# Performance work log

Measured on AMD Instinct MI355X. Metric: run time of the kernel, lower is better.

## Reference

```python
import jax, jax.numpy as jnp
import numpy as np

B, T, L, IN, D, H = 2, 16, 256, 768, 1024, 16
HD = D // H
NREG = 4
P = NREG + 2          # frozen prefix: registers + noise + action
DEPTH = 8
TINT = 4              # temporal_attention_interval
CTX = 30              # temporal_context_length
BASE = 1000.0         # rope_base
EPS = 1e-6            # qk_norm_eps / rmsnorm eps
HID = 4096            # 4.0 * latent_dim
S = L + P             # tokens per frame


def _rms(x, w=None, eps=EPS):
    y = x * jax.lax.rsqrt(jnp.mean(x * x, axis=-1, keepdims=True) + eps)
    return y * w if w is not None else y


def _rope_cache(n, hd, base):
    inv = base ** (-jnp.arange(0, hd, 2, dtype=jnp.float32) / hd)
    ang = jnp.arange(n, dtype=jnp.float32)[:, None] * inv[None, :]  # [n, hd/2]
    return jnp.cos(ang), jnp.sin(ang)


def _apply_rope(x, cos, sin):
    x1, x2 = x[..., ::2], x[..., 1::2]
    return jnp.stack([x1 * cos - x2 * sin, x1 * sin + x2 * cos], axis=-1).reshape(x.shape)


def _attn(x, Wqkv, Wo, cos, sin, mask):
    # x: [..., S, D]; mask: bool, True = attend, broadcastable to [..., H, S, S]
    qkv = x @ Wqkv
    q, k, v = jnp.split(qkv, 3, axis=-1)
    heads = lambda t: t.reshape(t.shape[:-1] + (H, HD)).swapaxes(-2, -3)  # [..., H, S, HD]
    q, k, v = heads(q), heads(k), heads(v)
    q = _apply_rope(_rms(q), cos, sin)   # qk-norm then RoPE
    k = _apply_rope(_rms(k), cos, sin)
    s = jnp.einsum('...qd,...kd->...qk', q, k) / jnp.sqrt(jnp.float32(HD))
    s = jnp.where(mask, s, jnp.float32(-1e9))
    p = jax.nn.softmax(s, axis=-1) * mask.any(axis=-1, keepdims=True)  # zero rows with no allowed keys
    o = jnp.einsum('...qk,...kd->...qd', p, v)
    return o.swapaxes(-2, -3).reshape(x.shape) @ Wo


def _spatial_mask():
    m = np.zeros((S, S), bool)
    r, n, a, ls = NREG, NREG, NREG + 1, NREG + 2
    m[ls:, ls:] = True; m[ls:, n] = True; m[ls:, a] = True; m[ls:, :r] = True
    m[n, n] = True; m[a, a] = True
    m[:r, ls:] = True; m[:r, n] = True; m[:r, a] = True; m[:r, :r] = True
    return jnp.asarray(m)


def _temporal_mask(indep):
    m = jnp.tril(jnp.ones((T, T), bool), -1)  # strictly-past causal
    if CTX is not None and CTX < T:
        m = m & jnp.triu(m, -CTX)             # sliding context window
    m = jnp.broadcast_to(m, (B, T, T))
    m = jnp.where(indep[:, None, None], False, m)
    return m[:, None, None]  # [B,1,1,T,T] -> broadcasts over token pos and heads


def setup_inputs() -> dict:
    key = jax.random.key(0)
    ks = iter(jax.random.split(key, 40))
    g = lambda shape, s=0.02: jax.random.normal(next(ks), shape, jnp.float32) * s
    inp = {
        'noisy_latents': jax.random.normal(next(ks), (B, T, L, IN), jnp.float32),
        'noise_levels': jax.random.uniform(next(ks), (B, T), jnp.float32),
        'actions': jax.random.normal(next(ks), (B, T, 6), jnp.float32),
        'independent_frames_mask': jnp.zeros((B,), bool),
        'actions_mask': jnp.ones((B, T), bool),
        'W_in': g((IN, D)),
        'noise_w1': g((1, D)), 'noise_b1': jnp.zeros((D,), jnp.float32),
        'noise_w2': g((D, D)), 'noise_b2': jnp.zeros((D,), jnp.float32),
        'base_action_embed': g((D,)),
        'action_w': g((6, D)), 'action_b': jnp.zeros((D,), jnp.float32),
        'registers': g((NREG, D)),
        'ln1_w': jnp.ones((DEPTH, D), jnp.float32),
        'Wqkv_s': g((DEPTH, D, 3 * D)), 'Wo_s': g((DEPTH, D, D)),
        'lnt_w': jnp.ones((DEPTH, D), jnp.float32),
        'Wqkv_t': g((DEPTH, D, 3 * D)), 'Wo_t': g((DEPTH, D, D)),
        'ln2_w': jnp.ones((DEPTH, D), jnp.float32),
        'W1': g((DEPTH, D, HID)), 'W2': g((DEPTH, D, HID)), 'W3': g((DEPTH, HID, D)),
        'final_w': jnp.ones((D,), jnp.float32),
        'W_out': g((D, IN)), 'b_out': jnp.zeros((IN,), jnp.float32),
    }
    return inp


def reference(noisy_latents, noise_levels, actions, independent_frames_mask, actions_mask,
              W_in, noise_w1, noise_b1, noise_w2, noise_b2, base_action_embed,
              action_w, action_b, registers, ln1_w, Wqkv_s, Wo_s, lnt_w, Wqkv_t, Wo_t,
              ln2_w, W1, W2, W3, final_w, W_out, b_out):
    noisy_tokens = noisy_latents @ W_in                                   # [B,T,L,D]
    base = jnp.broadcast_to(base_action_embed, (B, T, 1, D))
    act = base + (actions @ action_w + action_b)[:, :, None, :]
    act = jnp.where(actions_mask[:, :, None, None], act, base)            # [B,T,1,D]
    nz = jax.nn.silu(noise_levels[..., None] @ noise_w1 + noise_b1) @ noise_w2 + noise_b2
    nz = nz[:, :, None, :]                                                # [B,T,1,D]
    reg = jnp.broadcast_to(registers, (B, T, NREG, D))
    x = jnp.concatenate([reg, nz, act, noisy_tokens], axis=2)             # [B,T,S,D]

    sp_mask = _spatial_mask()
    tm_mask = _temporal_mask(independent_frames_mask)
    sp_cos, sp_sin = _rope_cache(S, HD, BASE)
    tm_cos, tm_sin = _rope_cache(T, HD, BASE)
    keep_tok = (jnp.arange(S) >= P)[None, :, None, None]                  # zero temporal update on frozen prefix

    for i in range(DEPTH):
        h = _rms(x, ln1_w[i])
        x = x + _attn(h, Wqkv_s[i], Wo_s[i], sp_cos, sp_sin, sp_mask)
        if i % TINT == 0:
            ht = _rms(x, lnt_w[i]).transpose(0, 2, 1, 3)                  # [B,S,T,D]
            ot = _attn(ht, Wqkv_t[i], Wo_t[i], tm_cos, tm_sin, tm_mask)
            x = x + (ot * keep_tok).transpose(0, 2, 1, 3)
        h2 = _rms(x, ln2_w[i])
        x = x + (jax.nn.silu(h2 @ W1[i]) * (h2 @ W2[i])) @ W3[i]

    latents = _rms(x[..., P:, :], final_w)
    pred_clean_latents = latents @ W_out + b_out                          # [B,T,L,IN]
    return pred_clean_latents
```

## Files before the change

kernel.cpp:

```cpp
#include <hip/hip_runtime.h>
#include <cstdint>
#include <cstddef>

#define DEV __device__ __forceinline__

typedef __attribute__((ext_vector_type(8))) __bf16 bf16x8;
typedef __attribute__((ext_vector_type(4))) float f32x4;

#define NTOK   8384
#define NTOKP  8448
#define NLAT   8192

DEV float b2f(unsigned short u) {
  unsigned int x = ((unsigned int)u) << 16;
  return __builtin_bit_cast(float, x);
}
DEV unsigned short f2b(float f) {
  unsigned int x = __builtin_bit_cast(unsigned int, f);
  x += 0x7fffu + ((x >> 16) & 1u);
  return (unsigned short)(x >> 16);
}
DEV float wred_sum(float v) {
#pragma unroll
  for (int o = 32; o; o >>= 1) v += __shfl_xor(v, o);
  return v;
}
DEV bool mask_or(const void* p, int i) {
  return ((const unsigned char*)p)[i] != 0 || ((const int*)p)[i] != 0;
}
DEV bool mask_and(const void* p, int i) {
  return ((const unsigned char*)p)[i] != 0 && ((const int*)p)[i] != 0;
}


__global__ void conv_f2b(const float* __restrict__ in, unsigned short* __restrict__ out, int n4) {
  int i = blockIdx.x * 256 + threadIdx.x;
  if (i < n4) {
    float4 v = ((const float4*)in)[i];
    ushort4 o;
    o.x = f2b(v.x); o.y = f2b(v.y); o.z = f2b(v.z); o.w = f2b(v.w);
    ((ushort4*)out)[i] = o;
  }
}

__global__ void build_rope(float2* __restrict__ out, int npos) {
  int idx = blockIdx.x * 256 + threadIdx.x;
  if (idx >= npos * 32) return;
  int pos = idx >> 5, i = idx & 31;
  float inv = powf(1000.0f, -(float)(2 * i) * (1.0f / 64.0f));
  float ang = (float)pos * inv;
  float sv, cv;
  sincosf(ang, &sv, &cv);
  out[idx] = make_float2(cv, sv);
}

__global__ __launch_bounds__(256) void transpose_w(const float* __restrict__ in,
                                                   unsigned short* __restrict__ out,
                                                   int K, int N, int ostride) {
  __shared__ float tile[32][33];
  int kb = blockIdx.x * 32, nb = blockIdx.y * 32;
  int tx = threadIdx.x & 31, ty = threadIdx.x >> 5;
#pragma unroll
  for (int i = 0; i < 32; i += 8)
    tile[ty + i][tx] = in[(size_t)(kb + ty + i) * N + (nb + tx)];
  __syncthreads();
#pragma unroll
  for (int i = 0; i < 32; i += 8)
    out[(size_t)(nb + ty + i) * ostride + (kb + tx)] = f2b(tile[tx][ty + i]);
}

__global__ __launch_bounds__(256) void noise_embed(const float* __restrict__ nlvl,
                                                   const float* __restrict__ w1,
                                                   const float* __restrict__ b1,
                                                   const float* __restrict__ w2,
                                                   const float* __restrict__ b2,
                                                   float* __restrict__ nz) {
  int bt = blockIdx.x, tid = threadIdx.x;
  __shared__ float h1[1024];
  float x = nlvl[bt];
  for (int d = tid; d < 1024; d += 256) {
    float v = x * w1[d] + b1[d];
    h1[d] = v / (1.0f + expf(-v));
  }
  __syncthreads();
  for (int dp = tid; dp < 1024; dp += 256) {
    float acc = b2[dp];
#pragma unroll 8
    for (int d = 0; d < 1024; ++d) acc += h1[d] * w2[(size_t)d * 1024 + dp];
    nz[(size_t)bt * 1024 + dp] = acc;
  }
}

__global__ void embed_special(float* __restrict__ x, const float* __restrict__ regs,
                              const float* __restrict__ nz, const float* __restrict__ base_emb,
                              const float* __restrict__ actions, const float* __restrict__ action_w,
                              const float* __restrict__ action_b,
                              const void* __restrict__ amask) {
  int bt = blockIdx.x, d = threadIdx.x;
  float* xr = x + (size_t)bt * 262 * 1024;
#pragma unroll
  for (int r = 0; r < 4; ++r) xr[r * 1024 + d] = regs[r * 1024 + d];
  xr[4 * 1024 + d] = nz[(size_t)bt * 1024 + d];
  float a = base_emb[d];
  if (mask_or(amask, bt)) {
    float s = action_b[d];
#pragma unroll
    for (int i = 0; i < 6; ++i) s += actions[bt * 6 + i] * action_w[i * 1024 + d];
    a += s;
  }
  xr[5 * 1024 + d] = a;
}

template <bool REMAP>
__global__ __launch_bounds__(256) void rms_k(const float* __restrict__ x,
                                             const float* __restrict__ w,
                                             unsigned short* __restrict__ out) {
  int m = blockIdx.x, tid = threadIdx.x;
  size_t src = REMAP ? ((size_t)(m >> 8) * 262 + 6 + (m & 255)) : (size_t)m;
  float4 v = ((const float4*)(x + src * 1024))[tid];
  float ss = v.x * v.x + v.y * v.y + v.z * v.z + v.w * v.w;
  ss = wred_sum(ss);
  __shared__ float sred[4];
  if ((tid & 63) == 0) sred[tid >> 6] = ss;
  __syncthreads();
  float tot = sred[0] + sred[1] + sred[2] + sred[3];
  float sc = rsqrtf(tot * (1.0f / 1024.0f) + 1e-6f);
  float4 wv = ((const float4*)w)[tid];
  ushort4 o;
  o.x = f2b(v.x * sc * wv.x); o.y = f2b(v.y * sc * wv.y);
  o.z = f2b(v.z * sc * wv.z); o.w = f2b(v.w * sc * wv.w);
  ((ushort4*)(out + (size_t)m * 1024))[tid] = o;
}

__global__ __launch_bounds__(256) void qk_rms_rope_f(float* __restrict__ qkv,
                                                     const float2* __restrict__ rope,
                                                     int temporal) {
  int gw = blockIdx.x * 4 + (threadIdx.x >> 6);
  int lane = threadIdx.x & 63;
  if (gw >= NTOK * 32) return;
  int qk = gw & 1, hh = (gw >> 1) & 15, tok = gw >> 5;
  int pos = temporal ? ((tok / 262) & 15) : (tok % 262);
  float* p = qkv + (size_t)tok * 3072 + qk * 1024 + hh * 64 + lane;
  float v = *p;
  float ss = wred_sum(v * v);
  v *= rsqrtf(ss * (1.0f / 64.0f) + 1e-6f);
  float partner = __shfl_xor(v, 1);
  float2 cs = rope[pos * 32 + (lane >> 1)];
  float outv = ((lane & 1) == 0) ? (v * cs.x - partner * cs.y)
                                 : (partner * cs.y + v * cs.x);
  *p = outv;
}

#define KSTR 72
#define VSTR 296
__global__ __launch_bounds__(256) void attn_spatial(const float* __restrict__ qkv,
                                                    unsigned short* __restrict__ o) {
  __shared__ unsigned short Ks[272 * KSTR];
  __shared__ unsigned short Vt[64 * VSTR];
  __shared__ unsigned short Ps[4][16 * VSTR];
  const int h = blockIdx.x & 15;
  const int bt = blockIdx.x >> 4;
  const int tid = threadIdx.x, wave = tid >> 6, lane = tid & 63;
  const size_t tb = (size_t)bt * 262;

  {
    const int d = lane;
#pragma unroll 1
    for (int pss = 0; pss < 17; ++pss) {
      const int t0 = (pss * 4 + wave) * 4;
      ushort4 vp;
      unsigned short* vpp = (unsigned short*)&vp;
#pragma unroll
      for (int j = 0; j < 4; ++j) {
        const int t = t0 + j;
        float kv = 0.f, vv = 0.f;
        if (t < 262) {
          const size_t rb = (tb + t) * 3072 + h * 64 + d;
          kv = qkv[rb + 1024];
          vv = qkv[rb + 2048];
        }
        Ks[t * KSTR + d] = f2b(kv);
        vpp[j] = f2b(vv);
      }
      *(ushort4*)(&Vt[d * VSTR + t0]) = vp;
    }
    for (int idx = tid; idx < 64 * 24; idx += 256) {
      Vt[(idx / 24) * VSTR + 272 + (idx % 24)] = 0;
    }
    for (int idx = tid; idx < 4 * 16 * 34; idx += 256) {
      int w = idx / (16 * 34), r = (idx / 34) & 15, c = idx % 34;
      Ps[w][r * VSTR + 262 + c] = 0;
    }
  }
  __syncthreads();

  unsigned short* Pw = &Ps[wave][0];
  const int kcol = lane & 15;
  const int g8 = (lane >> 4) << 3;
  const int rq = (lane >> 4) << 2;

#pragma unroll 1
  for (int qc = wave; qc < 17; qc += 4) {
    const int q0 = qc * 16;
    const int qrow = q0 + kcol;
    const int grow = qrow < 262 ? qrow : 261;
    const float* qp = qkv + (tb + grow) * 3072 + h * 64 + g8;
    bf16x8 aq0, aq1;
    {
      float4 a = *(const float4*)qp, b = *(const float4*)(qp + 4);
      float4 c = *(const float4*)(qp + 32), e = *(const float4*)(qp + 36);
      unsigned short* u0 = (unsigned short*)&aq0;
      unsigned short* u1 = (unsigned short*)&aq1;
      u0[0] = f2b(a.x); u0[1] = f2b(a.y); u0[2] = f2b(a.z); u0[3] = f2b(a.w);
      u0[4] = f2b(b.x); u0[5] = f2b(b.y); u0[6] = f2b(b.z); u0[7] = f2b(b.w);
      u1[0] = f2b(c.x); u1[1] = f2b(c.y); u1[2] = f2b(c.z); u1[3] = f2b(c.w);
      u1[4] = f2b(e.x); u1[5] = f2b(e.y); u1[6] = f2b(e.z); u1[7] = f2b(e.w);
    }
    f32x4 sc[17];
#pragma unroll
    for (int kc = 0; kc < 17; ++kc) {
      const unsigned short* kb = &Ks[(kc * 16 + kcol) * KSTR + g8];
      f32x4 z = {};
      z = __builtin_amdgcn_mfma_f32_16x16x32_bf16(aq0, *(const bf16x8*)kb, z, 0, 0, 0);
      sc[kc] = __builtin_amdgcn_mfma_f32_16x16x32_bf16(aq1, *(const bf16x8*)(kb + 32), z, 0, 0, 0);
    }
#pragma unroll
    for (int kc = 0; kc < 17; ++kc) {
      const int k = kc * 16 + kcol;
#pragma unroll
      for (int j = 0; j < 4; ++j) {
        const int sq = q0 + rq + j;
        const bool valid = (k < 262) && ((sq != 4 && sq != 5) || (k == sq));
        sc[kc][j] = valid ? sc[kc][j] * 0.125f : -1e30f;
      }
    }
    float mx[4], sm[4];
#pragma unroll
    for (int j = 0; j < 4; ++j) {
      float m = -1e30f;
#pragma unroll
      for (int kc = 0; kc < 17; ++kc) m = fmaxf(m, sc[kc][j]);
#pragma unroll
      for (int off = 1; off < 16; off <<= 1) m = fmaxf(m, __shfl_xor(m, off));
      mx[j] = m;
      float s = 0.f;
#pragma unroll
      for (int kc = 0; kc < 17; ++kc) {
        float e = expf(sc[kc][j] - m);
        sc[kc][j] = e;
        s += e;
      }
#pragma unroll
      for (int off = 1; off < 16; off <<= 1) s += __shfl_xor(s, off);
      sm[j] = 1.0f / s;
    }
#pragma unroll
    for (int kc = 0; kc < 17; ++kc) {
      const int k = kc * 16 + kcol;
#pragma unroll
      for (int j = 0; j < 4; ++j)
        Pw[(rq + j) * VSTR + k] = f2b(sc[kc][j] * sm[j]);
    }
    f32x4 oacc[4] = {};
#pragma unroll
    for (int tc = 0; tc < 9; ++tc) {
      const bf16x8 ap = *(const bf16x8*)(&Pw[kcol * VSTR + tc * 32 + g8]);
#pragma unroll
      for (int nt = 0; nt < 4; ++nt) {
        const bf16x8 bv = *(const bf16x8*)(&Vt[(nt * 16 + kcol) * VSTR + tc * 32 + g8]);
        oacc[nt] = __builtin_amdgcn_mfma_f32_16x16x32_bf16(ap, bv, oacc[nt], 0, 0, 0);
      }
    }
#pragma unroll
    for (int nt = 0; nt < 4; ++nt) {
#pragma unroll
      for (int j = 0; j < 4; ++j) {
        const int sq = q0 + rq + j;
        if (sq < 262)
          o[(tb + sq) * 1024 + h * 64 + nt * 16 + kcol] = f2b(oacc[nt][j]);
      }
    }
  }
}

__global__ __launch_bounds__(256) void attn_temporal(const float* __restrict__ qkv,
                                                     unsigned short* __restrict__ o,
                                                     const void* __restrict__ indep) {
  int gw = blockIdx.x * 4 + (threadIdx.x >> 6);
  int lane = threadIdx.x & 63;
  if (gw >= NTOK) return;
  int h = gw & 15;
  int s = (gw >> 4) % 262;
  int b = (gw >> 4) / 262;
  bool dead = (s < 6) || mask_and(indep, b);
  float q[16], kk[16], vv[16], out[16];
#pragma unroll
  for (int t = 0; t < 16; ++t) {
    out[t] = 0.f;
    if (!dead) {
      size_t off = ((size_t)((b * 16 + t) * 262 + s)) * 3072 + h * 64 + lane;
      q[t] = qkv[off];
      kk[t] = qkv[off + 1024];
      vv[t] = qkv[off + 2048];
    }
  }
  if (!dead) {
#pragma unroll
    for (int t = 1; t < 16; ++t) {
      float m = -1e30f, l = 0.f, acc = 0.f;
#pragma unroll
      for (int j = 0; j < t; ++j) {
        float pr = q[t] * kk[j];
#pragma unroll
        for (int o2 = 32; o2; o2 >>= 1) pr += __shfl_xor(pr, o2);
        pr *= 0.125f;
        float mn = fmaxf(m, pr);
        float cor = expf(m - mn);
        float e = expf(pr - mn);
        l = l * cor + e;
        acc = acc * cor + e * vv[j];
        m = mn;
      }
      out[t] = acc / l;
    }
  }
#pragma unroll
  for (int t = 0; t < 16; ++t) {
    size_t off = ((size_t)((b * 16 + t) * 262 + s)) * 1024 + h * 64 + lane;
    o[off] = f2b(out[t]);
  }
}

DEV void stage_tiles(const unsigned short* __restrict__ A, const unsigned short* __restrict__ Bw,
                     size_t arow0, size_t brow0, int K, int k0,
                     unsigned short* As, unsigned short* Bs, int wave, int lane) {
  const int srow = lane >> 2;
  const int scol = (lane & 3) * 8;
#pragma unroll
  for (int c = 0; c < 2; ++c) {
    const int chunk = wave * 2 + c;
    unsigned short* ga = const_cast<unsigned short*>(A + (arow0 + chunk * 16 + srow) * K + k0 + scol);
    unsigned short* gb = const_cast<unsigned short*>(Bw + (brow0 + chunk * 16 + srow) * K + k0 + scol);
    __builtin_amdgcn_global_load_lds((__attribute__((address_space(1))) void*)ga,
                                     (__attribute__((address_space(3))) void*)(As + chunk * 512),
                                     16, 0, 0);
    __builtin_amdgcn_global_load_lds((__attribute__((address_space(1))) void*)gb,
                                     (__attribute__((address_space(3))) void*)(Bs + chunk * 512),
                                     16, 0, 0);
  }
}

template <int EPI>
__global__ __launch_bounds__(256) void gemm_k(const unsigned short* __restrict__ A,
                                              const unsigned short* __restrict__ Bw,
                                              void* __restrict__ C,
                                              const float* __restrict__ aux,
                                              int Mvalid, int K, int ldc) {
  __shared__ unsigned short As[2][128 * 32];
  __shared__ unsigned short Bs[2][128 * 32];
  const int tid = threadIdx.x;
  const int wave = tid >> 6, lane = tid & 63;
  const int wm = wave >> 1, wn = wave & 1;
  const size_t arow0 = (size_t)blockIdx.x * 128;
  const size_t brow0 = (size_t)blockIdx.y * 128;

  f32x4 acc[4][4] = {};
  const int KT = K >> 5;

  stage_tiles(A, Bw, arow0, brow0, K, 0, As[0], Bs[0], wave, lane);
  __syncthreads();
  int buf = 0;
  for (int kt = 0; kt < KT; ++kt) {
    if (kt + 1 < KT)
      stage_tiles(A, Bw, arow0, brow0, K, (kt + 1) << 5, As[buf ^ 1], Bs[buf ^ 1], wave, lane);
    const int kk = (lane >> 4) * 8;
    const int rsel = lane & 15;
    bf16x8 af[4], bfr[4];
#pragma unroll
    for (int mt = 0; mt < 4; ++mt)
      af[mt] = *reinterpret_cast<const bf16x8*>(&As[buf][(wm * 64 + mt * 16 + rsel) * 32 + kk]);
#pragma unroll
    for (int nt = 0; nt < 4; ++nt)
      bfr[nt] = *reinterpret_cast<const bf16x8*>(&Bs[buf][(wn * 64 + nt * 16 + rsel) * 32 + kk]);
#pragma unroll
    for (int mt = 0; mt < 4; ++mt) {
#pragma unroll
      for (int nt = 0; nt < 4; ++nt)
        acc[mt][nt] = __builtin_amdgcn_mfma_f32_16x16x32_bf16(af[mt], bfr[nt], acc[mt][nt], 0, 0, 0);
    }
    __syncthreads();
    buf ^= 1;
  }

  const int row_base = blockIdx.x * 128 + wm * 64;
  const int col_base = blockIdx.y * 128 + wn * 64;
#pragma unroll
  for (int mt = 0; mt < 4; ++mt) {
#pragma unroll
    for (int nt = 0; nt < 4; ++nt) {
      const int col = col_base + nt * 16 + (lane & 15);
      const int r0 = row_base + mt * 16 + ((lane >> 4) << 2);
#pragma unroll
      for (int j = 0; j < 4; ++j) {
        const int row = r0 + j;
        float v = acc[mt][nt][j];
        if (EPI == 2) {
          float partner = __shfl_xor(v, 1);
          if (row < Mvalid && !(lane & 1)) {
            float sv = v / (1.0f + expf(-v));
            ((unsigned short*)C)[(size_t)row * ldc + (col >> 1)] = f2b(sv * partner);
          }
        } else if (row < Mvalid) {
          if (EPI == 0) {
            ((unsigned short*)C)[(size_t)row * ldc + col] = f2b(v);
          } else if (EPI == 1) {
            float* p = (float*)C + (size_t)row * ldc + col;
            *p += v;
          } else if (EPI == 3) {
            ((float*)C)[(size_t)row * ldc + col] = v + aux[col];
          } else if (EPI == 4) {
            ((float*)C)[(size_t)row * ldc + col] = v;
          } else if (EPI == 5) {
            int xr = (row >> 8) * 262 + 6 + (row & 255);
            ((float*)C)[(size_t)xr * ldc + col] = v;
          }
        }
      }
    }
  }
}

extern "C" void kernel_launch(void* const* d_in, const int* in_sizes, int n_in,
                              void* d_out, int out_size, void* d_ws, size_t ws_size,
                              hipStream_t stream) {
  const float* noisy = (const float*)d_in[0];
  const float* nlvl = (const float*)d_in[1];
  const float* actions = (const float*)d_in[2];
  const void* indep = d_in[3];
  const void* amask = d_in[4];
  const float* W_in = (const float*)d_in[5];
  const float* noise_w1 = (const float*)d_in[6];
  const float* noise_b1 = (const float*)d_in[7];
  const float* noise_w2 = (const float*)d_in[8];
  const float* noise_b2 = (const float*)d_in[9];
  const float* base_emb = (const float*)d_in[10];
  const float* action_w = (const float*)d_in[11];
  const float* action_b = (const float*)d_in[12];
  const float* registers = (const float*)d_in[13];
  const float* ln1_w = (const float*)d_in[14];
  const float* Wqkv_s = (const float*)d_in[15];
  const float* Wo_s = (const float*)d_in[16];
  const float* lnt_w = (const float*)d_in[17];
  const float* Wqkv_t = (const float*)d_in[18];
  const float* Wo_t = (const float*)d_in[19];
  const float* ln2_w = (const float*)d_in[20];
  const float* W1 = (const float*)d_in[21];
  const float* W2 = (const float*)d_in[22];
  const float* W3 = (const float*)d_in[23];
  const float* final_w = (const float*)d_in[24];
  const float* W_out = (const float*)d_in[25];
  const float* b_out = (const float*)d_in[26];

  char* p = (char*)d_ws;
  auto alloc = [&](size_t bytes) {
    char* r = p;
    p += (bytes + 255) & ~(size_t)255;
    return r;
  };
  float* X = (float*)alloc((size_t)NTOKP * 1024 * 4);
  unsigned short* HB = (unsigned short*)alloc((size_t)NTOKP * 1024 * 2);
  unsigned short* AO = (unsigned short*)alloc((size_t)NTOKP * 1024 * 2);
  char* SCR = alloc((size_t)NTOKP * 3072 * 4);
  float* QKV = (float*)SCR;
  unsigned short* G = (unsigned short*)SCR;
  unsigned short* NLB = (unsigned short*)SCR;
  float* NZ = (float*)alloc(32 * 1024 * 4);
  float2* RSP = (float2*)alloc(262 * 32 * 8);
  float2* RTM = (float2*)alloc(16 * 32 * 8);
  unsigned short* WINT = (unsigned short*)alloc((size_t)1024 * 768 * 2);
  unsigned short* WQKVS = (unsigned short*)alloc((size_t)8 * 3072 * 1024 * 2);
  unsigned short* WOS = (unsigned short*)alloc((size_t)8 * 1024 * 1024 * 2);
  unsigned short* WQKVT = (unsigned short*)alloc((size_t)8 * 3072 * 1024 * 2);
  unsigned short* WOT = (unsigned short*)alloc((size_t)8 * 1024 * 1024 * 2);
  unsigned short* W12T = (unsigned short*)alloc((size_t)8 * 8192 * 1024 * 2);
  unsigned short* W3T = (unsigned short*)alloc((size_t)8 * 1024 * 4096 * 2);
  unsigned short* WOUTT = (unsigned short*)alloc((size_t)768 * 1024 * 2);

  auto tr = [&](const float* in, unsigned short* out, int K, int N, int ostride) {
    dim3 g(K / 32, N / 32);
    transpose_w<<<g, 256, 0, stream>>>(in, out, K, N, ostride);
  };
  tr(W_in, WINT, 768, 1024, 768);
  for (int i = 0; i < 8; ++i) {
    tr(Wqkv_s + (size_t)i * 1024 * 3072, WQKVS + (size_t)i * 3072 * 1024, 1024, 3072, 1024);
    tr(Wo_s + (size_t)i * 1024 * 1024, WOS + (size_t)i * 1024 * 1024, 1024, 1024, 1024);
    tr(Wqkv_t + (size_t)i * 1024 * 3072, WQKVT + (size_t)i * 3072 * 1024, 1024, 3072, 1024);
    tr(Wo_t + (size_t)i * 1024 * 1024, WOT + (size_t)i * 1024 * 1024, 1024, 1024, 1024);
    tr(W1 + (size_t)i * 1024 * 4096, W12T + (size_t)i * 8192 * 1024, 1024, 4096, 2048);
    tr(W2 + (size_t)i * 1024 * 4096, W12T + (size_t)i * 8192 * 1024 + 1024, 1024, 4096, 2048);
    tr(W3 + (size_t)i * 4096 * 1024, W3T + (size_t)i * 1024 * 4096, 4096, 1024, 4096);
  }
  tr(W_out, WOUTT, 1024, 768, 1024);

  build_rope<<<33, 256, 0, stream>>>(RSP, 262);
  build_rope<<<2, 256, 0, stream>>>(RTM, 16);
  conv_f2b<<<6144, 256, 0, stream>>>(noisy, NLB, (NLAT * 768) / 4);
  noise_embed<<<32, 256, 0, stream>>>(nlvl, noise_w1, noise_b1, noise_w2, noise_b2, NZ);
  embed_special<<<32, 1024, 0, stream>>>(X, registers, NZ, base_emb, actions, action_w, action_b, amask);
  {
    dim3 g(64, 8);
    gemm_k<5><<<g, 256, 0, stream>>>(NLB, WINT, X, nullptr, NLAT, 768, 1024);
  }

  for (int i = 0; i < 8; ++i) {
    rms_k<false><<<NTOK, 256, 0, stream>>>(X, ln1_w + i * 1024, HB);
    {
      dim3 g(66, 24);
      gemm_k<4><<<g, 256, 0, stream>>>(HB, WQKVS + (size_t)i * 3072 * 1024, QKV, nullptr, NTOK, 1024, 3072);
    }
    qk_rms_rope_f<<<67072, 256, 0, stream>>>(QKV, RSP, 0);
    attn_spatial<<<512, 256, 0, stream>>>(QKV, AO);
    {
      dim3 g(66, 8);
      gemm_k<1><<<g, 256, 0, stream>>>(AO, WOS + (size_t)i * 1024 * 1024, X, nullptr, NTOK, 1024, 1024);
    }
    if ((i & 3) == 0) {
      rms_k<false><<<NTOK, 256, 0, stream>>>(X, lnt_w + i * 1024, HB);
      {
        dim3 g(66, 24);
        gemm_k<4><<<g, 256, 0, stream>>>(HB, WQKVT + (size_t)i * 3072 * 1024, QKV, nullptr, NTOK, 1024, 3072);
      }
      qk_rms_rope_f<<<67072, 256, 0, stream>>>(QKV, RTM, 1);
      attn_temporal<<<2096, 256, 0, stream>>>(QKV, AO, indep);
      {
        dim3 g(66, 8);
        gemm_k<1><<<g, 256, 0, stream>>>(AO, WOT + (size_t)i * 1024 * 1024, X, nullptr, NTOK, 1024, 1024);
      }
    }
    rms_k<false><<<NTOK, 256, 0, stream>>>(X, ln2_w + i * 1024, HB);
    {
      dim3 g(66, 64);
      gemm_k<2><<<g, 256, 0, stream>>>(HB, W12T + (size_t)i * 8192 * 1024, G, nullptr, NTOK, 1024, 4096);
    }
    {
      dim3 g(66, 8);
      gemm_k<1><<<g, 256, 0, stream>>>(G, W3T + (size_t)i * 1024 * 4096, X, nullptr, NTOK, 4096, 1024);
    }
  }

  rms_k<true><<<NLAT, 256, 0, stream>>>(X, final_w, HB);
  {
    dim3 g(64, 6);
    gemm_k<3><<<g, 256, 0, stream>>>(HB, WOUTT, d_out, b_out, NLAT, 1024, 768);
  }
}
```

Measured before the change: 6.506 ms.

## Fuse qk-norm and RoPE into attention kernels, store QKV in bf16, parallelize noise MLP

Drops the separate qk_rms_rope pass. Per-head RMS norm and RoPE are now applied inside the spatial and temporal attention kernels on Q and K as they are loaded. The QKV GEMM writes bf16 (mode 0) instead of fp32, halving QKV traffic and removing a full read-modify-write pass over the QKV buffer. The noise MLP is split into an elementwise kernel plus a K-split matmul with atomic adds, so it runs on more blocks. The trade-offs are bf16 rounding of Q/K before normalization and nondeterministic float atomics.

Result: faster. 6.225 ms (-4.3%).

```diff
diff --git a/kernel.cpp b/kernel.cpp
--- a/kernel.cpp
+++ b/kernel.cpp
@@ -69,26 +69,41 @@
     out[(size_t)(nb + ty + i) * ostride + (kb + tx)] = f2b(tile[tx][ty + i]);
 }
 
-__global__ __launch_bounds__(256) void noise_embed(const float* __restrict__ nlvl,
-                                                   const float* __restrict__ w1,
-                                                   const float* __restrict__ b1,
-                                                   const float* __restrict__ w2,
-                                                   const float* __restrict__ b2,
-                                                   float* __restrict__ nz) {
-  int bt = blockIdx.x, tid = threadIdx.x;
-  __shared__ float h1[1024];
-  float x = nlvl[bt];
-  for (int d = tid; d < 1024; d += 256) {
-    float v = x * w1[d] + b1[d];
-    h1[d] = v / (1.0f + expf(-v));
+__global__ __launch_bounds__(256) void noise_h1(const float* __restrict__ nlvl,
+                                                const float* __restrict__ w1,
+                                                const float* __restrict__ b1,
+                                                const float* __restrict__ b2,
+                                                float* __restrict__ h1,
+                                                float* __restrict__ nz) {
+  int i = blockIdx.x * 256 + threadIdx.x;
+  int bt = i >> 10, d = i & 1023;
+  float v = nlvl[bt] * w1[d] + b1[d];
+  h1[i] = v / (1.0f + expf(-v));
+  nz[i] = b2[d];
+}
+
+__global__ __launch_bounds__(256) void noise_mm(const float* __restrict__ h1,
+                                                const float* __restrict__ w2,
+                                                float* __restrict__ nz) {
+  __shared__ float hs[32][128];
+  int kc = blockIdx.x >> 4, dpg = blockIdx.x & 15;
+  int tid = threadIdx.x;
+  int k0 = kc * 128;
+  for (int idx = tid; idx < 32 * 128; idx += 256) {
+    int bt = idx >> 7, k = idx & 127;
+    hs[bt][k] = h1[bt * 1024 + k0 + k];
   }
   __syncthreads();
-  for (int dp = tid; dp < 1024; dp += 256) {
-    float acc = b2[dp];
-#pragma unroll 8
-    for (int d = 0; d < 1024; ++d) acc += h1[d] * w2[(size_t)d * 1024 + dp];
-    nz[(size_t)bt * 1024 + dp] = acc;
-  }
+  int dp = dpg * 64 + (tid & 63);
+  int bt0 = (tid >> 6) * 8;
+  float acc[8] = {};
+  for (int k = 0; k < 128; ++k) {
+    float w = w2[(size_t)(k0 + k) * 1024 + dp];
+#pragma unroll
+    for (int j = 0; j < 8; ++j) acc[j] += hs[bt0 + j][k] * w;
+  }
+#pragma unroll
+  for (int j = 0; j < 8; ++j) atomicAdd(&nz[(bt0 + j) * 1024 + dp], acc[j]);
 }
 
 __global__ void embed_special(float* __restrict__ x, const float* __restrict__ regs,
@@ -132,29 +147,11 @@
   ((ushort4*)(out + (size_t)m * 1024))[tid] = o;
 }
 
-__global__ __launch_bounds__(256) void qk_rms_rope_f(float* __restrict__ qkv,
-                                                     const float2* __restrict__ rope,
-                                                     int temporal) {
-  int gw = blockIdx.x * 4 + (threadIdx.x >> 6);
-  int lane = threadIdx.x & 63;
-  if (gw >= NTOK * 32) return;
-  int qk = gw & 1, hh = (gw >> 1) & 15, tok = gw >> 5;
-  int pos = temporal ? ((tok / 262) & 15) : (tok % 262);
-  float* p = qkv + (size_t)tok * 3072 + qk * 1024 + hh * 64 + lane;
-  float v = *p;
-  float ss = wred_sum(v * v);
-  v *= rsqrtf(ss * (1.0f / 64.0f) + 1e-6f);
-  float partner = __shfl_xor(v, 1);
-  float2 cs = rope[pos * 32 + (lane >> 1)];
-  float outv = ((lane & 1) == 0) ? (v * cs.x - partner * cs.y)
-                                 : (partner * cs.y + v * cs.x);
-  *p = outv;
-}
-
 #define KSTR 72
 #define VSTR 296
-__global__ __launch_bounds__(256) void attn_spatial(const float* __restrict__ qkv,
-                                                    unsigned short* __restrict__ o) {
+__global__ __launch_bounds__(256) void attn_spatial(const unsigned short* __restrict__ qkv,
+                                                    unsigned short* __restrict__ o,
+                                                    const float2* __restrict__ rope) {
   __shared__ unsigned short Ks[272 * KSTR];
   __shared__ unsigned short Vt[64 * VSTR];
   __shared__ unsigned short Ps[4][16 * VSTR];
@@ -176,9 +173,16 @@
         float kv = 0.f, vv = 0.f;
         if (t < 262) {
           const size_t rb = (tb + t) * 3072 + h * 64 + d;
-          kv = qkv[rb + 1024];
-          vv = qkv[rb + 2048];
+          kv = b2f(qkv[rb + 1024]);
+          vv = b2f(qkv[rb + 2048]);
         }
+        float ss = wred_sum(kv * kv);
+        kv *= rsqrtf(ss * (1.0f / 64.0f) + 1e-6f);
+        float partner = __shfl_xor(kv, 1);
+        const int tc = t < 262 ? t : 261;
+        float2 cs = rope[tc * 32 + (d >> 1)];
+        kv = ((d & 1) == 0) ? (kv * cs.x - partner * cs.y)
+                            : (partner * cs.y + kv * cs.x);
         Ks[t * KSTR + d] = f2b(kv);
         vpp[j] = f2b(vv);
       }
@@ -197,6 +201,7 @@
   unsigned short* Pw = &Ps[wave][0];
   const int kcol = lane & 15;
   const int g8 = (lane >> 4) << 3;
+  const int g4 = g8 >> 1;
   const int rq = (lane >> 4) << 2;
 
 #pragma unroll 1
@@ -204,17 +209,35 @@
     const int q0 = qc * 16;
     const int qrow = q0 + kcol;
     const int grow = qrow < 262 ? qrow : 261;
-    const float* qp = qkv + (tb + grow) * 3072 + h * 64 + g8;
+    const unsigned short* qp = qkv + (tb + grow) * 3072 + h * 64 + g8;
+    float qv[16];
+    {
+      ushort4 a = *(const ushort4*)qp, b = *(const ushort4*)(qp + 4);
+      ushort4 c = *(const ushort4*)(qp + 32), e = *(const ushort4*)(qp + 36);
+      qv[0] = b2f(a.x); qv[1] = b2f(a.y); qv[2] = b2f(a.z); qv[3] = b2f(a.w);
+      qv[4] = b2f(b.x); qv[5] = b2f(b.y); qv[6] = b2f(b.z); qv[7] = b2f(b.w);
+      qv[8] = b2f(c.x); qv[9] = b2f(c.y); qv[10] = b2f(c.z); qv[11] = b2f(c.w);
+      qv[12] = b2f(e.x); qv[13] = b2f(e.y); qv[14] = b2f(e.z); qv[15] = b2f(e.w);
+    }
+    float ss = 0.f;
+#pragma unroll
+    for (int i = 0; i < 16; ++i) ss += qv[i] * qv[i];
+    ss += __shfl_xor(ss, 16);
+    ss += __shfl_xor(ss, 32);
+    const float qsc = rsqrtf(ss * (1.0f / 64.0f) + 1e-6f);
     bf16x8 aq0, aq1;
-    {
-      float4 a = *(const float4*)qp, b = *(const float4*)(qp + 4);
-      float4 c = *(const float4*)(qp + 32), e = *(const float4*)(qp + 36);
-      unsigned short* u0 = (unsigned short*)&aq0;
-      unsigned short* u1 = (unsigned short*)&aq1;
-      u0[0] = f2b(a.x); u0[1] = f2b(a.y); u0[2] = f2b(a.z); u0[3] = f2b(a.w);
-      u0[4] = f2b(b.x); u0[5] = f2b(b.y); u0[6] = f2b(b.z); u0[7] = f2b(b.w);
-      u1[0] = f2b(c.x); u1[1] = f2b(c.y); u1[2] = f2b(c.z); u1[3] = f2b(c.w);
-      u1[4] = f2b(e.x); u1[5] = f2b(e.y); u1[6] = f2b(e.z); u1[7] = f2b(e.w);
+    unsigned short* u0 = (unsigned short*)&aq0;
+    unsigned short* u1 = (unsigned short*)&aq1;
+#pragma unroll
+    for (int i = 0; i < 4; ++i) {
+      float2 cs0 = rope[grow * 32 + g4 + i];
+      float a = qv[2 * i] * qsc, b = qv[2 * i + 1] * qsc;
+      u0[2 * i] = f2b(a * cs0.x - b * cs0.y);
+      u0[2 * i + 1] = f2b(a * cs0.y + b * cs0.x);
+      float2 cs1 = rope[grow * 32 + 16 + g4 + i];
+      float a1 = qv[8 + 2 * i] * qsc, b1 = qv[9 + 2 * i] * qsc;
+      u1[2 * i] = f2b(a1 * cs1.x - b1 * cs1.y);
+      u1[2 * i + 1] = f2b(a1 * cs1.y + b1 * cs1.x);
     }
     f32x4 sc[17];
 #pragma unroll
@@ -234,7 +257,7 @@
         sc[kc][j] = valid ? sc[kc][j] * 0.125f : -1e30f;
       }
     }
-    float mx[4], sm[4];
+    float sm[4];
 #pragma unroll
     for (int j = 0; j < 4; ++j) {
       float m = -1e30f;
@@ -242,7 +265,6 @@
       for (int kc = 0; kc < 17; ++kc) m = fmaxf(m, sc[kc][j]);
 #pragma unroll
       for (int off = 1; off < 16; off <<= 1) m = fmaxf(m, __shfl_xor(m, off));
-      mx[j] = m;
       float s = 0.f;
 #pragma unroll
       for (int kc = 0; kc < 17; ++kc) {
@@ -283,8 +305,9 @@
   }
 }
 
-__global__ __launch_bounds__(256) void attn_temporal(const float* __restrict__ qkv,
+__global__ __launch_bounds__(256) void attn_temporal(const unsigned short* __restrict__ qkv,
                                                      unsigned short* __restrict__ o,
+                                                     const float2* __restrict__ rope,
                                                      const void* __restrict__ indep) {
   int gw = blockIdx.x * 4 + (threadIdx.x >> 6);
   int lane = threadIdx.x & 63;
@@ -299,12 +322,24 @@
     out[t] = 0.f;
     if (!dead) {
       size_t off = ((size_t)((b * 16 + t) * 262 + s)) * 3072 + h * 64 + lane;
-      q[t] = qkv[off];
-      kk[t] = qkv[off + 1024];
-      vv[t] = qkv[off + 2048];
+      q[t] = b2f(qkv[off]);
+      kk[t] = b2f(qkv[off + 1024]);
+      vv[t] = b2f(qkv[off + 2048]);
     }
   }
   if (!dead) {
+#pragma unroll
+    for (int t = 0; t < 16; ++t) {
+      float sq_ = wred_sum(q[t] * q[t]);
+      float qv = q[t] * rsqrtf(sq_ * (1.0f / 64.0f) + 1e-6f);
+      float sk_ = wred_sum(kk[t] * kk[t]);
+      float kv = kk[t] * rsqrtf(sk_ * (1.0f / 64.0f) + 1e-6f);
+      float2 cs = rope[t * 32 + (lane >> 1)];
+      float qp = __shfl_xor(qv, 1);
+      float kp = __shfl_xor(kv, 1);
+      q[t] = ((lane & 1) == 0) ? (qv * cs.x - qp * cs.y) : (qp * cs.y + qv * cs.x);
+      kk[t] = ((lane & 1) == 0) ? (kv * cs.x - kp * cs.y) : (kp * cs.y + kv * cs.x);
+    }
 #pragma unroll
     for (int t = 1; t < 16; ++t) {
       float m = -1e30f, l = 0.f, acc = 0.f;
@@ -470,11 +505,12 @@
   float* X = (float*)alloc((size_t)NTOKP * 1024 * 4);
   unsigned short* HB = (unsigned short*)alloc((size_t)NTOKP * 1024 * 2);
   unsigned short* AO = (unsigned short*)alloc((size_t)NTOKP * 1024 * 2);
-  char* SCR = alloc((size_t)NTOKP * 3072 * 4);
-  float* QKV = (float*)SCR;
+  char* SCR = alloc((size_t)NTOKP * 4096 * 2);
+  unsigned short* QKV = (unsigned short*)SCR;
   unsigned short* G = (unsigned short*)SCR;
   unsigned short* NLB = (unsigned short*)SCR;
   float* NZ = (float*)alloc(32 * 1024 * 4);
+  float* H1 = (float*)alloc(32 * 1024 * 4);
   float2* RSP = (float2*)alloc(262 * 32 * 8);
   float2* RTM = (float2*)alloc(16 * 32 * 8);
   unsigned short* WINT = (unsigned short*)alloc((size_t)1024 * 768 * 2);
@@ -505,7 +541,8 @@
   build_rope<<<33, 256, 0, stream>>>(RSP, 262);
   build_rope<<<2, 256, 0, stream>>>(RTM, 16);
   conv_f2b<<<6144, 256, 0, stream>>>(noisy, NLB, (NLAT * 768) / 4);
-  noise_embed<<<32, 256, 0, stream>>>(nlvl, noise_w1, noise_b1, noise_w2, noise_b2, NZ);
+  noise_h1<<<128, 256, 0, stream>>>(nlvl, noise_w1, noise_b1, noise_b2, H1, NZ);
+  noise_mm<<<128, 256, 0, stream>>>(H1, noise_w2, NZ);
   embed_special<<<32, 1024, 0, stream>>>(X, registers, NZ, base_emb, actions, action_w, action_b, amask);
   {
     dim3 g(64, 8);
@@ -516,10 +553,9 @@
     rms_k<false><<<NTOK, 256, 0, stream>>>(X, ln1_w + i * 1024, HB);
     {
       dim3 g(66, 24);
-      gemm_k<4><<<g, 256, 0, stream>>>(HB, WQKVS + (size_t)i * 3072 * 1024, QKV, nullptr, NTOK, 1024, 3072);
-    }
-    qk_rms_rope_f<<<67072, 256, 0, stream>>>(QKV, RSP, 0);
-    attn_spatial<<<512, 256, 0, stream>>>(QKV, AO);
+      gemm_k<0><<<g, 256, 0, stream>>>(HB, WQKVS + (size_t)i * 3072 * 1024, QKV, nullptr, NTOK, 1024, 3072);
+    }
+    attn_spatial<<<512, 256, 0, stream>>>(QKV, AO, RSP);
     {
       dim3 g(66, 8);
       gemm_k<1><<<g, 256, 0, stream>>>(AO, WOS + (size_t)i * 1024 * 1024, X, nullptr, NTOK, 1024, 1024);
@@ -528,10 +564,9 @@
       rms_k<false><<<NTOK, 256, 0, stream>>>(X, lnt_w + i * 1024, HB);
       {
         dim3 g(66, 24);
-        gemm_k<4><<<g, 256, 0, stream>>>(HB, WQKVT + (size_t)i * 3072 * 1024, QKV, nullptr, NTOK, 1024, 3072);
-      }
-      qk_rms_rope_f<<<67072, 256, 0, stream>>>(QKV, RTM, 1);
-      attn_temporal<<<2096, 256, 0, stream>>>(QKV, AO, indep);
+        gemm_k<0><<<g, 256, 0, stream>>>(HB, WQKVT + (size_t)i * 3072 * 1024, QKV, nullptr, NTOK, 1024, 3072);
+      }
+      attn_temporal<<<2096, 256, 0, stream>>>(QKV, AO, RTM, indep);
       {
         dim3 g(66, 8);
         gemm_k<1><<<g, 256, 0, stream>>>(AO, WOT + (size_t)i * 1024 * 1024, X, nullptr, NTOK, 1024, 1024);
```
